# Optimization experiments

Measured on AMD Instinct MI355X. Metric: run time of the kernel, lower is better.

The kernel has to match this reference:

```python
import jax, jax.numpy as jnp
import numpy as np

DIM = 512
NUM_HEADS = 8
HEAD_DIM = DIM // NUM_HEADS
EPS = 1e-6


def setup_inputs() -> dict:
    key = jax.random.key(0)
    k_x, k_qkv, k_out, k_b = jax.random.split(key, 4)
    B, N = 8, 4096
    x = jax.random.normal(k_x, (B, N, DIM), dtype=jnp.float32)
    # nn.Linear weights stored as [out_features, in_features]; we keep [in, out] for x @ W
    s_qkv = 1.0 / np.sqrt(DIM)
    W_qkv = jax.random.uniform(k_qkv, (DIM, 3 * DIM), minval=-s_qkv, maxval=s_qkv, dtype=jnp.float32)
    W_out = jax.random.uniform(k_out, (DIM, DIM), minval=-s_qkv, maxval=s_qkv, dtype=jnp.float32)
    b_out = jax.random.uniform(k_b, (DIM,), minval=-s_qkv, maxval=s_qkv, dtype=jnp.float32)
    return {"x": x, "W_qkv": W_qkv, "W_out": W_out, "b_out": b_out}


def _feature_map(x):
    # elu(x) + 1
    return jax.nn.elu(x) + 1.0


def reference(x, W_qkv, W_out, b_out):
    B, N, C = x.shape
    H, D = NUM_HEADS, HEAD_DIM
    qkv = x @ W_qkv                              # [B, N, 3C]
    qkv = qkv.reshape(B, N, 3, H, D).transpose(2, 0, 3, 1, 4)  # [3, B, H, N, D]
    q, k, v = qkv[0], qkv[1], qkv[2]
    q_phi = _feature_map(q)                      # [B, H, N, D]
    k_phi = _feature_map(k)
    KV = jnp.einsum('bhnd,bhne->bhde', k_phi, v)  # [B, H, D, D]
    K_sum = k_phi.sum(axis=2)                     # [B, H, D]
    denom = jnp.einsum('bhnd,bhd->bhn', q_phi, K_sum)[..., None] + EPS  # [B, H, N, 1]
    out = jnp.einsum('bhnd,bhde->bhne', q_phi, KV) / denom              # [B, H, N, D]
    out = out.transpose(0, 2, 1, 3).reshape(B, N, C)
    return out @ W_out + b_out
```

## Files before the change

### kernel.cpp

```cpp
#include <hip/hip_runtime.h>
#include <stdint.h>

typedef float    f32x4 __attribute__((ext_vector_type(4)));
typedef short    s16x8 __attribute__((ext_vector_type(8)));
typedef short    s16x4 __attribute__((ext_vector_type(4)));
typedef unsigned short u16;
typedef uint32_t u32;

#define DEVINL __device__ __forceinline__

DEVINL float bf2f(u16 u) { union { u32 i; float f; } x; x.i = ((u32)u) << 16; return x.f; }
DEVINL u16 f2bf(float f) {
  union { float f; u32 i; } x; x.f = f;
  u32 i = x.i;
  return (u16)((i + 0x7FFFu + ((i >> 16) & 1u)) >> 16);
}

DEVINL void gload16(const void* g, void* l) {
  __builtin_amdgcn_global_load_lds((const __attribute__((address_space(1))) void*)g,
                                   (__attribute__((address_space(3))) void*)l,
                                   16, 0, 0);
}

__global__ __launch_bounds__(256) void k_conv_bf16(const float* __restrict__ x,
                                                   u16* __restrict__ xb, int n8) {
  int stride = gridDim.x * blockDim.x;
  for (int i = blockIdx.x * blockDim.x + threadIdx.x; i < n8; i += stride) {
    const f32x4* p = (const f32x4*)(x + (size_t)i * 8);
    f32x4 a = p[0], b = p[1];
    s16x8 o;
    o[0] = (short)f2bf(a[0]); o[1] = (short)f2bf(a[1]);
    o[2] = (short)f2bf(a[2]); o[3] = (short)f2bf(a[3]);
    o[4] = (short)f2bf(b[0]); o[5] = (short)f2bf(b[1]);
    o[6] = (short)f2bf(b[2]); o[7] = (short)f2bf(b[3]);
    *(s16x8*)(xb + (size_t)i * 8) = o;
  }
}

__global__ __launch_bounds__(256) void k_transpose_bf16(const float* __restrict__ W,
                                                        u16* __restrict__ Wt, int K, int N) {
  __shared__ __align__(16) float t[64][65];
  int nb = N >> 6;
  int tn = blockIdx.x % nb, tk = blockIdx.x / nb;
  int n0 = tn << 6, k0 = tk << 6;
  int tid = threadIdx.x;
  int cr = tid >> 4, cc = (tid & 15) << 2;
#pragma unroll
  for (int i = 0; i < 4; i++) {
    int r = cr + (i << 4);
    f32x4 v = *(const f32x4*)(W + (size_t)(k0 + r) * N + n0 + cc);
    t[r][cc] = v[0]; t[r][cc + 1] = v[1]; t[r][cc + 2] = v[2]; t[r][cc + 3] = v[3];
  }
  __syncthreads();
#pragma unroll
  for (int i = 0; i < 4; i++) {
    int nn = cr + (i << 4);
    s16x4 o;
    o[0] = (short)f2bf(t[cc    ][nn]);
    o[1] = (short)f2bf(t[cc + 1][nn]);
    o[2] = (short)f2bf(t[cc + 2][nn]);
    o[3] = (short)f2bf(t[cc + 3][nn]);
    *(s16x4*)(Wt + (size_t)(n0 + nn) * K + k0 + cc) = o;
  }
}

template <int EPI>
__global__ __launch_bounds__(512, 1) void k_gemm(
    const u16* __restrict__ A, const u16* __restrict__ Bt,
    int nbn,
    u16* __restrict__ qph, u16* __restrict__ kph, u16* __restrict__ vv,
    float* __restrict__ out, const float* __restrict__ bias) {
  __shared__ __align__(16) u16 lsA[3][256 * 32];
  __shared__ __align__(16) u16 lsB[3][256 * 32];

  int nwg = gridDim.x;
  int bx = blockIdx.x;
  int o = (bx & 7) * (nwg >> 3) + (bx >> 3);
  int bm = o / nbn, bn = o % nbn;
  int m0 = bm << 8, n0 = bn << 8;
  int tid = threadIdx.x;
  int w = tid >> 6, lane = tid & 63;
  int lnlo = lane & 15, lnhi = lane >> 4;
  int wr = w >> 2, wc = w & 3;

  const u16* gAp[2]; const u16* gBp[2]; int ldst[2];
#pragma unroll
  for (int i = 0; i < 2; i++) {
    int c = tid + i * 512;
    int row = c >> 2, ch = c & 3;
    int gch = ch ^ ((row >> 1) & 3);
    gAp[i] = A + (size_t)(m0 + row) * 512 + gch * 8;
    gBp[i] = Bt + (size_t)(n0 + row) * 512 + gch * 8;
    ldst[i] = c * 8;
  }

  int offA[8], offB[4];
#pragma unroll
  for (int f = 0; f < 8; f++) {
    int r = wr * 128 + f * 16 + lnlo;
    offA[f] = r * 32 + (lnhi ^ ((r >> 1) & 3)) * 8;
  }
#pragma unroll
  for (int f = 0; f < 4; f++) {
    int r = wc * 64 + f * 16 + lnlo;
    offB[f] = r * 32 + (lnhi ^ ((r >> 1) & 3)) * 8;
  }

  f32x4 acc[8][4] = {};

#pragma unroll
  for (int i = 0; i < 2; i++) gload16(gAp[i], &lsA[0][ldst[i]]);
#pragma unroll
  for (int i = 0; i < 2; i++) gload16(gBp[i], &lsB[0][ldst[i]]);
#pragma unroll
  for (int i = 0; i < 2; i++) gload16(gAp[i] + 32, &lsA[1][ldst[i]]);
#pragma unroll
  for (int i = 0; i < 2; i++) gload16(gBp[i] + 32, &lsB[1][ldst[i]]);
  asm volatile("s_waitcnt vmcnt(4)" ::: "memory");
  __builtin_amdgcn_s_barrier();

#pragma unroll
  for (int t = 0; t < 16; t++) {
    int buf = t % 3;
    const u16* La = &lsA[buf][0];
    const u16* Lb = &lsB[buf][0];
    int k2 = (t + 2) * 32;
    int b2 = (t + 2) % 3;

    s16x8 bf[4], af[4];
#pragma unroll
    for (int f = 0; f < 4; f++) bf[f] = *(const s16x8*)(Lb + offB[f]);
#pragma unroll
    for (int f = 0; f < 4; f++) af[f] = *(const s16x8*)(La + offA[f]);
    if (t < 14) {
#pragma unroll
      for (int i = 0; i < 2; i++) gload16(gAp[i] + k2, &lsA[b2][ldst[i]]);
    }
    __builtin_amdgcn_s_barrier();
    __builtin_amdgcn_s_setprio(1);
#pragma unroll
    for (int mf = 0; mf < 4; mf++)
#pragma unroll
      for (int nf = 0; nf < 4; nf++)
        acc[mf][nf] = __builtin_amdgcn_mfma_f32_16x16x32_bf16(af[mf], bf[nf], acc[mf][nf], 0, 0, 0);
    __builtin_amdgcn_s_setprio(0);
    __builtin_amdgcn_s_barrier();

    s16x8 af2[4];
#pragma unroll
    for (int f = 0; f < 4; f++) af2[f] = *(const s16x8*)(La + offA[4 + f]);
    if (t < 14) {
#pragma unroll
      for (int i = 0; i < 2; i++) gload16(gBp[i] + k2, &lsB[b2][ldst[i]]);
    }
    __builtin_amdgcn_s_barrier();
    __builtin_amdgcn_s_setprio(1);
#pragma unroll
    for (int mf = 0; mf < 4; mf++)
#pragma unroll
      for (int nf = 0; nf < 4; nf++)
        acc[4 + mf][nf] = __builtin_amdgcn_mfma_f32_16x16x32_bf16(af2[mf], bf[nf], acc[4 + mf][nf], 0, 0, 0);
    __builtin_amdgcn_s_setprio(0);
    if (t <= 13)      asm volatile("s_waitcnt vmcnt(4)" ::: "memory");
    else if (t == 14) asm volatile("s_waitcnt vmcnt(0)" ::: "memory");
    if (t < 15) __builtin_amdgcn_s_barrier();
  }

  int gmB = m0 + wr * 128;
  int gnB = n0 + wc * 64;
  if (EPI == 0) {
#pragma unroll
    for (int mf = 0; mf < 8; mf++) {
#pragma unroll
      for (int nf = 0; nf < 4; nf++) {
        int col = gnB + nf * 16 + lnlo;
        int sec = col >> 9;
        int hh = (col >> 6) & 7;
        int dd = col & 63;
        u16* dst = (sec == 0) ? qph : ((sec == 1) ? kph : vv);
#pragma unroll
        for (int r = 0; r < 4; r++) {
          int rowm = gmB + mf * 16 + lnhi * 4 + r;
          float val = acc[mf][nf][r];
          if (sec < 2) val = (val > 0.f) ? (val + 1.f) : __expf(val);
          int bidx = rowm >> 12, tok = rowm & 4095;
          dst[(((size_t)(bidx * 8 + hh) * 4096 + tok) << 6) + dd] = f2bf(val);
        }
      }
    }
  } else {
#pragma unroll
    for (int mf = 0; mf < 8; mf++) {
#pragma unroll
      for (int nf = 0; nf < 4; nf++) {
        int col = gnB + nf * 16 + lnlo;
        float bv = bias[col];
#pragma unroll
        for (int r = 0; r < 4; r++) {
          int rowm = gmB + mf * 16 + lnhi * 4 + r;
          out[(size_t)rowm * 512 + col] = acc[mf][nf][r] + bv;
        }
      }
    }
  }
}

__global__ __launch_bounds__(256) void k_kv(const u16* __restrict__ kphi,
                                            const u16* __restrict__ vbuf,
                                            float* __restrict__ kvpart,
                                            float* __restrict__ kspart) {
  __shared__ __align__(16) float kf[16][64];
  __shared__ __align__(16) float vf[16][64];
  int bx = blockIdx.x;
  int bh = bx >> 4, ck = bx & 15;
  int tid = threadIdx.x;
  size_t base = ((size_t)bh * 4096 + ck * 256) * 64;
  float acc[4][4] = {};
  float ks[4] = {0.f, 0.f, 0.f, 0.f};
  int dq = tid >> 4, eq = tid & 15;
  int d0 = dq * 4, e0 = eq * 4;
  int half = tid >> 7;
  int t2 = tid & 127;
  int srow = t2 >> 3, sch = t2 & 7;

  for (int step = 0; step < 16; step++) {
    {
      const u16* src = (half ? vbuf : kphi) + base + (size_t)(step * 16 + srow) * 64 + sch * 8;
      s16x8 v8 = *(const s16x8*)src;
      float* dst = (half ? &vf[0][0] : &kf[0][0]) + srow * 64 + sch * 8;
      f32x4 lo = {bf2f((u16)v8[0]), bf2f((u16)v8[1]), bf2f((u16)v8[2]), bf2f((u16)v8[3])};
      f32x4 hi = {bf2f((u16)v8[4]), bf2f((u16)v8[5]), bf2f((u16)v8[6]), bf2f((u16)v8[7])};
      *(f32x4*)dst = lo;
      *(f32x4*)(dst + 4) = hi;
    }
    __syncthreads();
#pragma unroll
    for (int tk = 0; tk < 16; tk++) {
      f32x4 kq = *(const f32x4*)&kf[tk][d0];
      f32x4 vq = *(const f32x4*)&vf[tk][e0];
#pragma unroll
      for (int i = 0; i < 4; i++)
#pragma unroll
        for (int j = 0; j < 4; j++) acc[i][j] += kq[i] * vq[j];
      if (eq == 0) {
#pragma unroll
        for (int i = 0; i < 4; i++) ks[i] += kq[i];
      }
    }
    __syncthreads();
  }
  size_t pb = (size_t)(bh * 16 + ck) * 4096;
#pragma unroll
  for (int i = 0; i < 4; i++) {
    f32x4 o = {acc[i][0], acc[i][1], acc[i][2], acc[i][3]};
    *(f32x4*)(kvpart + pb + (size_t)(d0 + i) * 64 + e0) = o;
  }
  if (eq == 0) {
    f32x4 o = {ks[0], ks[1], ks[2], ks[3]};
    *(f32x4*)(kspart + (size_t)(bh * 16 + ck) * 64 + d0) = o;
  }
}

__global__ __launch_bounds__(256) void k_kvred(const float* __restrict__ kvpart,
                                               const float* __restrict__ kspart,
                                               u16* __restrict__ kvt_sw,
                                               float* __restrict__ ksum) {
  int bh = blockIdx.x;
  int tid = threadIdx.x;
  int e = tid >> 2, d0 = (tid & 3) * 16;
  size_t pb = (size_t)bh * 16 * 4096;
#pragma unroll
  for (int dd = 0; dd < 16; dd++) {
    int d = d0 + dd;
    float s = 0.f;
#pragma unroll
    for (int c = 0; c < 16; c++) s += kvpart[pb + (size_t)c * 4096 + d * 64 + e];
    int chs = (d >> 3) ^ (e & 7);
    kvt_sw[((size_t)bh * 64 + e) * 64 + chs * 8 + (d & 7)] = f2bf(s);
  }
  if (tid < 64) {
    float s = 0.f;
#pragma unroll
    for (int c = 0; c < 16; c++) s += kspart[(size_t)bh * 1024 + c * 64 + tid];
    ksum[bh * 64 + tid] = s;
  }
}

__global__ __launch_bounds__(256, 2) void k_attnout(const u16* __restrict__ qphi,
                                                    const u16* __restrict__ kvt_sw,
                                                    const float* __restrict__ ksum,
                                                    u16* __restrict__ y) {
  __shared__ __align__(16) u16 qa[256 * 64];
  __shared__ __align__(16) u16 bb[64 * 64];
  __shared__ float ksl[64];
  __shared__ float rdnl[256];
  int bx = blockIdx.x;
  int bh = bx >> 4, tch = bx & 15;
  int b = bh >> 3, hh = bh & 7;
  int tid = threadIdx.x, w = tid >> 6, lane = tid & 63;
  int lnlo = lane & 15, lnhi = lane >> 4;
  size_t qbase = ((size_t)bh * 4096 + tch * 256) * 64;

#pragma unroll
  for (int i = 0; i < 8; i++) {
    int c = i * 256 + tid;
    int row = c >> 3, ch = c & 7;
    int gcol = (ch ^ (row & 7)) << 3;
    gload16(qphi + qbase + (size_t)row * 64 + gcol, &qa[c * 8]);
  }
#pragma unroll
  for (int i = 0; i < 2; i++) {
    int c = i * 256 + tid;
    gload16(kvt_sw + (size_t)bh * 4096 + c * 8, &bb[c * 8]);
  }
  if (tid < 64) ksl[tid] = ksum[bh * 64 + tid];
  __syncthreads();

  {
    float den = 0.f;
#pragma unroll
    for (int ch = 0; ch < 8; ch++) {
      s16x8 v8 = *(const s16x8*)&qa[tid * 64 + ((ch ^ (tid & 7)) << 3)];
#pragma unroll
      for (int j = 0; j < 8; j++) den += bf2f((u16)v8[j]) * ksl[ch * 8 + j];
    }
    rdnl[tid] = 1.f / (den + 1e-6f);
  }
  __syncthreads();

  f32x4 acc[4][4] = {};
#pragma unroll
  for (int kk = 0; kk < 2; kk++) {
    s16x8 af[4], bfr[4];
#pragma unroll
    for (int f = 0; f < 4; f++) {
      int ra = w * 64 + f * 16 + lnlo;
      int ca = (kk * 4 + lnhi) ^ (ra & 7);
      af[f] = *(const s16x8*)&qa[ra * 64 + ca * 8];
      int rb = f * 16 + lnlo;
      int cb = (kk * 4 + lnhi) ^ (rb & 7);
      bfr[f] = *(const s16x8*)&bb[rb * 64 + cb * 8];
    }
#pragma unroll
    for (int mf = 0; mf < 4; mf++)
#pragma unroll
      for (int nf = 0; nf < 4; nf++)
        acc[mf][nf] = __builtin_amdgcn_mfma_f32_16x16x32_bf16(af[mf], bfr[nf], acc[mf][nf], 0, 0, 0);
  }

  size_t yrow0 = (size_t)b * 4096 + tch * 256;
#pragma unroll
  for (int mf = 0; mf < 4; mf++) {
#pragma unroll
    for (int nf = 0; nf < 4; nf++) {
      int e = nf * 16 + lnlo;
#pragma unroll
      for (int r = 0; r < 4; r++) {
        int tl = w * 64 + mf * 16 + lnhi * 4 + r;
        float val = acc[mf][nf][r] * rdnl[tl];
        y[(yrow0 + tl) * 512 + hh * 64 + e] = f2bf(val);
      }
    }
  }
}

#define OFF_XB     ((size_t)0)
#define OFF_WQKVT  ((size_t)33554432)
#define OFF_WOUTT  ((size_t)35127296)
#define OFF_QPHI   ((size_t)35651584)
#define OFF_KPHI   ((size_t)69206016)
#define OFF_VBUF   ((size_t)102760448)
#define OFF_KVPART ((size_t)136314880)
#define OFF_KSPART ((size_t)153092096)
#define OFF_KVT    ((size_t)153354240)
#define OFF_KSUM   ((size_t)153878528)

extern "C" void kernel_launch(void* const* d_in, const int* in_sizes, int n_in,
                              void* d_out, int out_size, void* d_ws, size_t ws_size,
                              hipStream_t stream) {
  const float* x    = (const float*)d_in[0];
  const float* Wqkv = (const float*)d_in[1];
  const float* Wout = (const float*)d_in[2];
  const float* bout = (const float*)d_in[3];
  float* out = (float*)d_out;
  char* ws = (char*)d_ws;

  u16* xb     = (u16*)(ws + OFF_XB);
  u16* y      = (u16*)(ws + OFF_XB);
  u16* wqkvt  = (u16*)(ws + OFF_WQKVT);
  u16* woutt  = (u16*)(ws + OFF_WOUTT);
  u16* qphi   = (u16*)(ws + OFF_QPHI);
  u16* kphi   = (u16*)(ws + OFF_KPHI);
  u16* vbuf   = (u16*)(ws + OFF_VBUF);
  float* kvpart = (float*)(ws + OFF_KVPART);
  float* kspart = (float*)(ws + OFF_KSPART);
  u16* kvt_sw = (u16*)(ws + OFF_KVT);
  float* ksum = (float*)(ws + OFF_KSUM);

  k_conv_bf16<<<2048, 256, 0, stream>>>(x, xb, 16777216 / 8);
  k_transpose_bf16<<<(1536 / 64) * (512 / 64), 256, 0, stream>>>(Wqkv, wqkvt, 512, 1536);
  k_transpose_bf16<<<(512 / 64) * (512 / 64), 256, 0, stream>>>(Wout, woutt, 512, 512);

  k_gemm<0><<<768, 512, 0, stream>>>(xb, wqkvt, 6, qphi, kphi, vbuf, nullptr, nullptr);
  k_kv<<<64 * 16, 256, 0, stream>>>(kphi, vbuf, kvpart, kspart);
  k_kvred<<<64, 256, 0, stream>>>(kvpart, kspart, kvt_sw, ksum);
  k_attnout<<<64 * 16, 256, 0, stream>>>(qphi, kvt_sw, ksum, y);
  k_gemm<1><<<256, 512, 0, stream>>>(y, woutt, 2, nullptr, nullptr, nullptr, out, bout);
}
```

Before: 178.5 us.

## Fuse fp32-to-bf16 conversion of x into QKV GEMM loads

Removes the separate x conversion kernel and adds a dedicated QKV GEMM that loads fp32 x through registers, converts to bf16, and stores into double-buffered LDS, replacing the direct global-to-LDS triple-buffered pipeline. This avoids writing and re-reading a bf16 copy of x, but the GEMM now reads fp32 A, which is twice the bytes, and A is re-read by each of the 6 column tiles. It also uses a simpler register-staged pipeline that may overlap less well. Separately, the k_kv inner loop is restructured to batch LDS loads four rows at a time.

```diff
diff --git a/kernel.cpp b/kernel.cpp
--- a/kernel.cpp
+++ b/kernel.cpp
@@ -8,6 +8,7 @@
 typedef uint32_t u32;
 
 #define DEVINL __device__ __forceinline__
+#define CFENCE asm volatile("" ::: "memory")
 
 DEVINL float bf2f(u16 u) { union { u32 i; float f; } x; x.i = ((u32)u) << 16; return x.f; }
 DEVINL u16 f2bf(float f) {
@@ -20,21 +21,6 @@
   __builtin_amdgcn_global_load_lds((const __attribute__((address_space(1))) void*)g,
                                    (__attribute__((address_space(3))) void*)l,
                                    16, 0, 0);
-}
-
-__global__ __launch_bounds__(256) void k_conv_bf16(const float* __restrict__ x,
-                                                   u16* __restrict__ xb, int n8) {
-  int stride = gridDim.x * blockDim.x;
-  for (int i = blockIdx.x * blockDim.x + threadIdx.x; i < n8; i += stride) {
-    const f32x4* p = (const f32x4*)(x + (size_t)i * 8);
-    f32x4 a = p[0], b = p[1];
-    s16x8 o;
-    o[0] = (short)f2bf(a[0]); o[1] = (short)f2bf(a[1]);
-    o[2] = (short)f2bf(a[2]); o[3] = (short)f2bf(a[3]);
-    o[4] = (short)f2bf(b[0]); o[5] = (short)f2bf(b[1]);
-    o[6] = (short)f2bf(b[2]); o[7] = (short)f2bf(b[3]);
-    *(s16x8*)(xb + (size_t)i * 8) = o;
-  }
 }
 
 __global__ __launch_bounds__(256) void k_transpose_bf16(const float* __restrict__ W,
@@ -61,6 +47,120 @@
     o[2] = (short)f2bf(t[cc + 2][nn]);
     o[3] = (short)f2bf(t[cc + 3][nn]);
     *(s16x4*)(Wt + (size_t)(n0 + nn) * K + k0 + cc) = o;
+  }
+}
+
+__global__ __launch_bounds__(512, 1) void k_gemm1(
+    const float* __restrict__ A, const u16* __restrict__ Bt, int nbn,
+    u16* __restrict__ qph, u16* __restrict__ kph, u16* __restrict__ vv) {
+  __shared__ __align__(16) u16 lsA[2][256 * 32];
+  __shared__ __align__(16) u16 lsB[2][256 * 32];
+
+  int nwg = gridDim.x, bx = blockIdx.x;
+  int o = (bx & 7) * (nwg >> 3) + (bx >> 3);
+  int bm = o / nbn, bn = o % nbn;
+  int m0 = bm << 8, n0 = bn << 8;
+  int tid = threadIdx.x, w = tid >> 6, lane = tid & 63;
+  int lnlo = lane & 15, lnhi = lane >> 4;
+  int wr = w >> 2, wc = w & 3;
+
+  const float* gAf[2]; const u16* gBp[2]; int ldst[2];
+#pragma unroll
+  for (int i = 0; i < 2; i++) {
+    int c = tid + i * 512, row = c >> 2, ch = c & 3;
+    int gch = ch ^ ((row >> 1) & 3);
+    gAf[i] = A + (size_t)(m0 + row) * 512 + gch * 8;
+    gBp[i] = Bt + (size_t)(n0 + row) * 512 + gch * 8;
+    ldst[i] = c * 8;
+  }
+  int offA[8], offB[4];
+#pragma unroll
+  for (int f = 0; f < 8; f++) { int r = wr * 128 + f * 16 + lnlo; offA[f] = r * 32 + (lnhi ^ ((r >> 1) & 3)) * 8; }
+#pragma unroll
+  for (int f = 0; f < 4; f++) { int r = wc * 64 + f * 16 + lnlo; offB[f] = r * 32 + (lnhi ^ ((r >> 1) & 3)) * 8; }
+
+  f32x4 rA[2][2]; s16x8 rB[2];
+  f32x4 acc[8][4] = {};
+
+#pragma unroll
+  for (int i = 0; i < 2; i++) {
+    const float* s = gAf[i];
+    rA[i][0] = *(const f32x4*)s; rA[i][1] = *(const f32x4*)(s + 4);
+    rB[i] = *(const s16x8*)gBp[i];
+  }
+#pragma unroll
+  for (int i = 0; i < 2; i++) {
+    s16x8 oo;
+#pragma unroll
+    for (int j = 0; j < 4; j++) { oo[j] = (short)f2bf(rA[i][0][j]); oo[4 + j] = (short)f2bf(rA[i][1][j]); }
+    *(s16x8*)&lsA[0][ldst[i]] = oo;
+    *(s16x8*)&lsB[0][ldst[i]] = rB[i];
+  }
+  asm volatile("s_waitcnt lgkmcnt(0)" ::: "memory");
+  __builtin_amdgcn_s_barrier();
+  CFENCE;
+
+#pragma unroll
+  for (int t = 0; t < 16; t++) {
+    const int par = t & 1;
+    if (t < 15) {
+      int k1 = (t + 1) * 32;
+#pragma unroll
+      for (int i = 0; i < 2; i++) {
+        const float* s = gAf[i] + k1;
+        rA[i][0] = *(const f32x4*)s; rA[i][1] = *(const f32x4*)(s + 4);
+        rB[i] = *(const s16x8*)(gBp[i] + k1);
+      }
+    }
+    CFENCE;
+    s16x8 af[8], bf[4];
+#pragma unroll
+    for (int f = 0; f < 4; f++) bf[f] = *(const s16x8*)&lsB[par][offB[f]];
+#pragma unroll
+    for (int f = 0; f < 8; f++) af[f] = *(const s16x8*)&lsA[par][offA[f]];
+    __builtin_amdgcn_s_setprio(1);
+#pragma unroll
+    for (int mf = 0; mf < 8; mf++)
+#pragma unroll
+      for (int nf = 0; nf < 4; nf++)
+        acc[mf][nf] = __builtin_amdgcn_mfma_f32_16x16x32_bf16(af[mf], bf[nf], acc[mf][nf], 0, 0, 0);
+    __builtin_amdgcn_s_setprio(0);
+    if (t < 15) {
+#pragma unroll
+      for (int i = 0; i < 2; i++) {
+        s16x8 oo;
+#pragma unroll
+        for (int j = 0; j < 4; j++) { oo[j] = (short)f2bf(rA[i][0][j]); oo[4 + j] = (short)f2bf(rA[i][1][j]); }
+        *(s16x8*)&lsA[par ^ 1][ldst[i]] = oo;
+        *(s16x8*)&lsB[par ^ 1][ldst[i]] = rB[i];
+      }
+      asm volatile("s_waitcnt lgkmcnt(0)" ::: "memory");
+      CFENCE;
+      __builtin_amdgcn_s_barrier();
+      CFENCE;
+    }
+  }
+
+  int gmB = m0 + wr * 128;
+  int gnB = n0 + wc * 64;
+#pragma unroll
+  for (int mf = 0; mf < 8; mf++) {
+#pragma unroll
+    for (int nf = 0; nf < 4; nf++) {
+      int col = gnB + nf * 16 + lnlo;
+      int sec = col >> 9;
+      int hh = (col >> 6) & 7;
+      int dd = col & 63;
+      u16* dst = (sec == 0) ? qph : ((sec == 1) ? kph : vv);
+#pragma unroll
+      for (int r = 0; r < 4; r++) {
+        int rowm = gmB + mf * 16 + lnhi * 4 + r;
+        float val = acc[mf][nf][r];
+        if (sec < 2) val = (val > 0.f) ? (val + 1.f) : __expf(val);
+        int bidx = rowm >> 12, tok = rowm & 4095;
+        dst[(((size_t)(bidx * 8 + hh) * 4096 + tok) << 6) + dd] = f2bf(val);
+      }
+    }
   }
 }
 
@@ -168,38 +268,16 @@
 
   int gmB = m0 + wr * 128;
   int gnB = n0 + wc * 64;
-  if (EPI == 0) {
-#pragma unroll
-    for (int mf = 0; mf < 8; mf++) {
-#pragma unroll
-      for (int nf = 0; nf < 4; nf++) {
-        int col = gnB + nf * 16 + lnlo;
-        int sec = col >> 9;
-        int hh = (col >> 6) & 7;
-        int dd = col & 63;
-        u16* dst = (sec == 0) ? qph : ((sec == 1) ? kph : vv);
-#pragma unroll
-        for (int r = 0; r < 4; r++) {
-          int rowm = gmB + mf * 16 + lnhi * 4 + r;
-          float val = acc[mf][nf][r];
-          if (sec < 2) val = (val > 0.f) ? (val + 1.f) : __expf(val);
-          int bidx = rowm >> 12, tok = rowm & 4095;
-          dst[(((size_t)(bidx * 8 + hh) * 4096 + tok) << 6) + dd] = f2bf(val);
-        }
-      }
-    }
-  } else {
-#pragma unroll
-    for (int mf = 0; mf < 8; mf++) {
-#pragma unroll
-      for (int nf = 0; nf < 4; nf++) {
-        int col = gnB + nf * 16 + lnlo;
-        float bv = bias[col];
-#pragma unroll
-        for (int r = 0; r < 4; r++) {
-          int rowm = gmB + mf * 16 + lnhi * 4 + r;
-          out[(size_t)rowm * 512 + col] = acc[mf][nf][r] + bv;
-        }
+#pragma unroll
+  for (int mf = 0; mf < 8; mf++) {
+#pragma unroll
+    for (int nf = 0; nf < 4; nf++) {
+      int col = gnB + nf * 16 + lnlo;
+      float bv = bias[col];
+#pragma unroll
+      for (int r = 0; r < 4; r++) {
+        int rowm = gmB + mf * 16 + lnhi * 4 + r;
+        out[(size_t)rowm * 512 + col] = acc[mf][nf][r] + bv;
       }
     }
   }
@@ -235,16 +313,23 @@
     }
     __syncthreads();
 #pragma unroll
-    for (int tk = 0; tk < 16; tk++) {
-      f32x4 kq = *(const f32x4*)&kf[tk][d0];
-      f32x4 vq = *(const f32x4*)&vf[tk][e0];
-#pragma unroll
-      for (int i = 0; i < 4; i++)
-#pragma unroll
-        for (int j = 0; j < 4; j++) acc[i][j] += kq[i] * vq[j];
-      if (eq == 0) {
-#pragma unroll
-        for (int i = 0; i < 4; i++) ks[i] += kq[i];
+    for (int tkb = 0; tkb < 4; tkb++) {
+      f32x4 kq[4], vq[4];
+#pragma unroll
+      for (int j = 0; j < 4; j++) {
+        kq[j] = *(const f32x4*)&kf[tkb * 4 + j][d0];
+        vq[j] = *(const f32x4*)&vf[tkb * 4 + j][e0];
+      }
+#pragma unroll
+      for (int j = 0; j < 4; j++) {
+#pragma unroll
+        for (int i = 0; i < 4; i++)
+#pragma unroll
+          for (int l = 0; l < 4; l++) acc[i][l] += kq[j][i] * vq[j][l];
+        if (eq == 0) {
+#pragma unroll
+          for (int i = 0; i < 4; i++) ks[i] += kq[j][i];
+        }
       }
     }
     __syncthreads();
@@ -364,7 +449,7 @@
   }
 }
 
-#define OFF_XB     ((size_t)0)
+#define OFF_Y      ((size_t)0)
 #define OFF_WQKVT  ((size_t)33554432)
 #define OFF_WOUTT  ((size_t)35127296)
 #define OFF_QPHI   ((size_t)35651584)
@@ -385,8 +470,7 @@
   float* out = (float*)d_out;
   char* ws = (char*)d_ws;
 
-  u16* xb     = (u16*)(ws + OFF_XB);
-  u16* y      = (u16*)(ws + OFF_XB);
+  u16* y      = (u16*)(ws + OFF_Y);
   u16* wqkvt  = (u16*)(ws + OFF_WQKVT);
   u16* woutt  = (u16*)(ws + OFF_WOUTT);
   u16* qphi   = (u16*)(ws + OFF_QPHI);
@@ -397,11 +481,10 @@
   u16* kvt_sw = (u16*)(ws + OFF_KVT);
   float* ksum = (float*)(ws + OFF_KSUM);
 
-  k_conv_bf16<<<2048, 256, 0, stream>>>(x, xb, 16777216 / 8);
   k_transpose_bf16<<<(1536 / 64) * (512 / 64), 256, 0, stream>>>(Wqkv, wqkvt, 512, 1536);
   k_transpose_bf16<<<(512 / 64) * (512 / 64), 256, 0, stream>>>(Wout, woutt, 512, 512);
 
-  k_gemm<0><<<768, 512, 0, stream>>>(xb, wqkvt, 6, qphi, kphi, vbuf, nullptr, nullptr);
+  k_gemm1<<<768, 512, 0, stream>>>(x, wqkvt, 6, qphi, kphi, vbuf);
   k_kv<<<64 * 16, 256, 0, stream>>>(kphi, vbuf, kvpart, kspart);
   k_kvred<<<64, 256, 0, stream>>>(kvpart, kspart, kvt_sw, ksum);
   k_attnout<<<64 * 16, 256, 0, stream>>>(qphi, kvt_sw, ksum, y);
```

Result: slower. 197.3 us (+10.5%).

## Stage GEMM and attention epilogues through LDS for vectorized 16-byte stores

Applied to the files above, without the earlier changes.

The QKV GEMM epilogue and the attention output epilogue now write bf16 results into shared memory first. They then read them back as contiguous 8-element vectors, so each thread issues wide coalesced global stores instead of scattered 2-byte stores. The KV accumulation loop is also restructured to batch four k/v loads before the FMAs, improving instruction-level parallelism. The cost is extra LDS traffic, more barriers per row fragment, and a reliance on the per-wave ebuf region not being read by other waves. The attention epilogue synchronises only with lgkmcnt waits and no barrier, which is valid only if each wave uses just its own slice.

```diff
diff --git a/kernel.cpp b/kernel.cpp
--- a/kernel.cpp
+++ b/kernel.cpp
@@ -8,6 +8,7 @@
 typedef uint32_t u32;
 
 #define DEVINL __device__ __forceinline__
+#define CFENCE asm volatile("" ::: "memory")
 
 DEVINL float bf2f(u16 u) { union { u32 i; float f; } x; x.i = ((u32)u) << 16; return x.f; }
 DEVINL u16 f2bf(float f) {
@@ -166,29 +167,43 @@
     if (t < 15) __builtin_amdgcn_s_barrier();
   }
 
-  int gmB = m0 + wr * 128;
-  int gnB = n0 + wc * 64;
   if (EPI == 0) {
+    __syncthreads();
+    u16* ebuf = &lsA[0][0];
+    const int EROW = 272;
+    int sec = n0 >> 9;
+    u16* dstE = (sec == 0) ? qph : ((sec == 1) ? kph : vv);
+    bool isphi = (sec < 2);
+    int erow = tid >> 4;
+    int ecol = (tid & 15) << 4;
+    int rowm = m0 + ((erow >> 4) << 7) + (erow & 15);
+    int col = n0 + ecol;
+    int hh = (col >> 6) & 7, dd = col & 63;
 #pragma unroll
     for (int mf = 0; mf < 8; mf++) {
 #pragma unroll
-      for (int nf = 0; nf < 4; nf++) {
-        int col = gnB + nf * 16 + lnlo;
-        int sec = col >> 9;
-        int hh = (col >> 6) & 7;
-        int dd = col & 63;
-        u16* dst = (sec == 0) ? qph : ((sec == 1) ? kph : vv);
+      for (int nf = 0; nf < 4; nf++)
 #pragma unroll
         for (int r = 0; r < 4; r++) {
-          int rowm = gmB + mf * 16 + lnhi * 4 + r;
           float val = acc[mf][nf][r];
-          if (sec < 2) val = (val > 0.f) ? (val + 1.f) : __expf(val);
-          int bidx = rowm >> 12, tok = rowm & 4095;
-          dst[(((size_t)(bidx * 8 + hh) * 4096 + tok) << 6) + dd] = f2bf(val);
+          if (isphi) val = (val > 0.f) ? (val + 1.f) : __expf(val);
+          ebuf[(wr * 16 + lnhi * 4 + r) * EROW + wc * 64 + nf * 16 + lnlo] = f2bf(val);
         }
+      __syncthreads();
+      {
+        int rm = rowm + mf * 16;
+        int bidx = rm >> 12, tok = rm & 4095;
+        size_t base = (((size_t)(bidx * 8 + hh) * 4096 + tok) << 6) + dd;
+        s16x8 v0 = *(const s16x8*)&ebuf[erow * EROW + ecol];
+        s16x8 v1 = *(const s16x8*)&ebuf[erow * EROW + ecol + 8];
+        *(s16x8*)&dstE[base] = v0;
+        *(s16x8*)&dstE[base + 8] = v1;
       }
+      __syncthreads();
     }
   } else {
+    int gmB = m0 + wr * 128;
+    int gnB = n0 + wc * 64;
 #pragma unroll
     for (int mf = 0; mf < 8; mf++) {
 #pragma unroll
@@ -235,29 +250,36 @@
     }
     __syncthreads();
 #pragma unroll
-    for (int tk = 0; tk < 16; tk++) {
-      f32x4 kq = *(const f32x4*)&kf[tk][d0];
-      f32x4 vq = *(const f32x4*)&vf[tk][e0];
-#pragma unroll
-      for (int i = 0; i < 4; i++)
-#pragma unroll
-        for (int j = 0; j < 4; j++) acc[i][j] += kq[i] * vq[j];
-      if (eq == 0) {
-#pragma unroll
-        for (int i = 0; i < 4; i++) ks[i] += kq[i];
+    for (int tkb = 0; tkb < 4; tkb++) {
+      f32x4 kq[4], vq[4];
+#pragma unroll
+      for (int j = 0; j < 4; j++) {
+        kq[j] = *(const f32x4*)&kf[tkb * 4 + j][d0];
+        vq[j] = *(const f32x4*)&vf[tkb * 4 + j][e0];
       }
+#pragma unroll
+      for (int j = 0; j < 4; j++) {
+#pragma unroll
+        for (int i = 0; i < 4; i++)
+#pragma unroll
+          for (int l = 0; l < 4; l++) acc[i][l] += kq[j][i] * vq[j][l];
+        if (eq == 0) {
+#pragma unroll
+          for (int i = 0; i < 4; i++) ks[i] += kq[j][i];
+        }
+      }
     }
     __syncthreads();
   }
   size_t pb = (size_t)(bh * 16 + ck) * 4096;
 #pragma unroll
   for (int i = 0; i < 4; i++) {
-    f32x4 o = {acc[i][0], acc[i][1], acc[i][2], acc[i][3]};
-    *(f32x4*)(kvpart + pb + (size_t)(d0 + i) * 64 + e0) = o;
+    f32x4 oo = {acc[i][0], acc[i][1], acc[i][2], acc[i][3]};
+    *(f32x4*)(kvpart + pb + (size_t)(d0 + i) * 64 + e0) = oo;
   }
   if (eq == 0) {
-    f32x4 o = {ks[0], ks[1], ks[2], ks[3]};
-    *(f32x4*)(kspart + (size_t)(bh * 16 + ck) * 64 + d0) = o;
+    f32x4 oo = {ks[0], ks[1], ks[2], ks[3]};
+    *(f32x4*)(kspart + (size_t)(bh * 16 + ck) * 64 + d0) = oo;
   }
 }
 
@@ -348,19 +370,30 @@
         acc[mf][nf] = __builtin_amdgcn_mfma_f32_16x16x32_bf16(af[mf], bfr[nf], acc[mf][nf], 0, 0, 0);
   }
 
+  u16* ebuf = &qa[w * 4096];
+  const int AROW = 72;
+  int erow = lane >> 2, echunk = (lane & 3) << 4;
   size_t yrow0 = (size_t)b * 4096 + tch * 256;
 #pragma unroll
   for (int mf = 0; mf < 4; mf++) {
 #pragma unroll
-    for (int nf = 0; nf < 4; nf++) {
-      int e = nf * 16 + lnlo;
+    for (int nf = 0; nf < 4; nf++)
 #pragma unroll
       for (int r = 0; r < 4; r++) {
         int tl = w * 64 + mf * 16 + lnhi * 4 + r;
         float val = acc[mf][nf][r] * rdnl[tl];
-        y[(yrow0 + tl) * 512 + hh * 64 + e] = f2bf(val);
+        ebuf[(lnhi * 4 + r) * AROW + nf * 16 + lnlo] = f2bf(val);
       }
-    }
+    asm volatile("s_waitcnt lgkmcnt(0)" ::: "memory");
+    {
+      int tok = w * 64 + mf * 16 + erow;
+      size_t dst = (yrow0 + tok) * 512 + hh * 64 + echunk;
+      s16x8 v0 = *(const s16x8*)&ebuf[erow * AROW + echunk];
+      s16x8 v1 = *(const s16x8*)&ebuf[erow * AROW + echunk + 8];
+      *(s16x8*)&y[dst] = v0;
+      *(s16x8*)&y[dst + 8] = v1;
+    }
+    asm volatile("s_waitcnt lgkmcnt(0)" ::: "memory");
   }
 }
 
```

New measurement: 184.9 us. 1.04x slower.

## Store K/V transposed and compute KV partials with MFMA; merge prep kernels

Applied to the files above, without the earlier changes.

The QKV GEMM epilogue now writes phi(K) and V in a transposed [bh, d, token] layout using 8-byte vector stores. This lets the KV-accumulation kernel stage whole 64x256 tiles into swizzled LDS with direct global-to-LDS loads and compute K^T V with bf16 MFMA instead of scalar FP32 FMAs. The three prep kernels (x conversion and two weight transposes) are merged into one launch. The transposed stores are strided across tokens, which may cost some write efficiency in the GEMM epilogue.

```diff
diff --git a/kernel.cpp b/kernel.cpp
--- a/kernel.cpp
+++ b/kernel.cpp
@@ -22,28 +22,36 @@
                                    16, 0, 0);
 }
 
-__global__ __launch_bounds__(256) void k_conv_bf16(const float* __restrict__ x,
-                                                   u16* __restrict__ xb, int n8) {
-  int stride = gridDim.x * blockDim.x;
-  for (int i = blockIdx.x * blockDim.x + threadIdx.x; i < n8; i += stride) {
-    const f32x4* p = (const f32x4*)(x + (size_t)i * 8);
-    f32x4 a = p[0], b = p[1];
-    s16x8 o;
-    o[0] = (short)f2bf(a[0]); o[1] = (short)f2bf(a[1]);
-    o[2] = (short)f2bf(a[2]); o[3] = (short)f2bf(a[3]);
-    o[4] = (short)f2bf(b[0]); o[5] = (short)f2bf(b[1]);
-    o[6] = (short)f2bf(b[2]); o[7] = (short)f2bf(b[3]);
-    *(s16x8*)(xb + (size_t)i * 8) = o;
-  }
-}
-
-__global__ __launch_bounds__(256) void k_transpose_bf16(const float* __restrict__ W,
-                                                        u16* __restrict__ Wt, int K, int N) {
+__global__ __launch_bounds__(256) void k_prep(const float* __restrict__ x,
+                                              u16* __restrict__ xb,
+                                              const float* __restrict__ Wqkv,
+                                              u16* __restrict__ wqkvt,
+                                              const float* __restrict__ Wout,
+                                              u16* __restrict__ woutt) {
   __shared__ __align__(16) float t[64][65];
+  int b = blockIdx.x;
+  int tid = threadIdx.x;
+  if (b < 2048) {
+    const int n8 = 2097152;
+    int stride = 2048 * 256;
+    for (int i = b * 256 + tid; i < n8; i += stride) {
+      const f32x4* p = (const f32x4*)(x + (size_t)i * 8);
+      f32x4 a = p[0], c = p[1];
+      s16x8 o;
+      o[0] = (short)f2bf(a[0]); o[1] = (short)f2bf(a[1]);
+      o[2] = (short)f2bf(a[2]); o[3] = (short)f2bf(a[3]);
+      o[4] = (short)f2bf(c[0]); o[5] = (short)f2bf(c[1]);
+      o[6] = (short)f2bf(c[2]); o[7] = (short)f2bf(c[3]);
+      *(s16x8*)(xb + (size_t)i * 8) = o;
+    }
+    return;
+  }
+  const float* W; u16* Wt; int K, N, tb;
+  if (b < 2048 + 192) { W = Wqkv; Wt = wqkvt; K = 512; N = 1536; tb = b - 2048; }
+  else               { W = Wout; Wt = woutt; K = 512; N = 512;  tb = b - 2240; }
   int nb = N >> 6;
-  int tn = blockIdx.x % nb, tk = blockIdx.x / nb;
+  int tn = tb % nb, tk = tb / nb;
   int n0 = tn << 6, k0 = tk << 6;
-  int tid = threadIdx.x;
   int cr = tid >> 4, cc = (tid & 15) << 2;
 #pragma unroll
   for (int i = 0; i < 4; i++) {
@@ -68,7 +76,7 @@
 __global__ __launch_bounds__(512, 1) void k_gemm(
     const u16* __restrict__ A, const u16* __restrict__ Bt,
     int nbn,
-    u16* __restrict__ qph, u16* __restrict__ kph, u16* __restrict__ vv,
+    u16* __restrict__ qph, u16* __restrict__ kphT, u16* __restrict__ vT,
     float* __restrict__ out, const float* __restrict__ bias) {
   __shared__ __align__(16) u16 lsA[3][256 * 32];
   __shared__ __align__(16) u16 lsB[3][256 * 32];
@@ -169,22 +177,45 @@
   int gmB = m0 + wr * 128;
   int gnB = n0 + wc * 64;
   if (EPI == 0) {
-#pragma unroll
-    for (int mf = 0; mf < 8; mf++) {
-#pragma unroll
-      for (int nf = 0; nf < 4; nf++) {
-        int col = gnB + nf * 16 + lnlo;
-        int sec = col >> 9;
-        int hh = (col >> 6) & 7;
-        int dd = col & 63;
-        u16* dst = (sec == 0) ? qph : ((sec == 1) ? kph : vv);
-#pragma unroll
-        for (int r = 0; r < 4; r++) {
-          int rowm = gmB + mf * 16 + lnhi * 4 + r;
-          float val = acc[mf][nf][r];
-          if (sec < 2) val = (val > 0.f) ? (val + 1.f) : __expf(val);
-          int bidx = rowm >> 12, tok = rowm & 4095;
-          dst[(((size_t)(bidx * 8 + hh) * 4096 + tok) << 6) + dd] = f2bf(val);
+    int sec = n0 >> 9;
+    if (sec == 0) {
+#pragma unroll
+      for (int mf = 0; mf < 8; mf++) {
+#pragma unroll
+        for (int nf = 0; nf < 4; nf++) {
+          int col = gnB + nf * 16 + lnlo;
+          int hh = (col >> 6) & 7;
+          int dd = col & 63;
+#pragma unroll
+          for (int r = 0; r < 4; r++) {
+            int rowm = gmB + mf * 16 + lnhi * 4 + r;
+            float val = acc[mf][nf][r];
+            val = (val > 0.f) ? (val + 1.f) : __expf(val);
+            int bidx = rowm >> 12, tok = rowm & 4095;
+            qph[(((size_t)(bidx * 8 + hh) * 4096 + tok) << 6) + dd] = f2bf(val);
+          }
+        }
+      }
+    } else {
+      u16* dstT = (sec == 1) ? kphT : vT;
+      bool isphi = (sec == 1);
+#pragma unroll
+      for (int mf = 0; mf < 8; mf++) {
+        int rowm = gmB + mf * 16 + lnhi * 4;
+        int bidx = rowm >> 12, tok = rowm & 4095;
+#pragma unroll
+        for (int nf = 0; nf < 4; nf++) {
+          int col = gnB + nf * 16 + lnlo;
+          int hh = (col >> 6) & 7;
+          int dd = col & 63;
+          s16x4 o4;
+#pragma unroll
+          for (int r = 0; r < 4; r++) {
+            float val = acc[mf][nf][r];
+            if (isphi) val = (val > 0.f) ? (val + 1.f) : __expf(val);
+            o4[r] = (short)f2bf(val);
+          }
+          *(s16x4*)&dstT[((size_t)(bidx * 8 + hh) * 64 + dd) * 4096 + tok] = o4;
         }
       }
     }
@@ -205,60 +236,72 @@
   }
 }
 
-__global__ __launch_bounds__(256) void k_kv(const u16* __restrict__ kphi,
-                                            const u16* __restrict__ vbuf,
-                                            float* __restrict__ kvpart,
-                                            float* __restrict__ kspart) {
-  __shared__ __align__(16) float kf[16][64];
-  __shared__ __align__(16) float vf[16][64];
+__global__ __launch_bounds__(256, 2) void k_kv(const u16* __restrict__ kphT,
+                                               const u16* __restrict__ vT,
+                                               float* __restrict__ kvpart,
+                                               float* __restrict__ kspart) {
+  __shared__ __align__(16) u16 lsK[64 * 256];
+  __shared__ __align__(16) u16 lsV[64 * 256];
+  __shared__ float red[4][64];
   int bx = blockIdx.x;
   int bh = bx >> 4, ck = bx & 15;
-  int tid = threadIdx.x;
-  size_t base = ((size_t)bh * 4096 + ck * 256) * 64;
-  float acc[4][4] = {};
-  float ks[4] = {0.f, 0.f, 0.f, 0.f};
-  int dq = tid >> 4, eq = tid & 15;
-  int d0 = dq * 4, e0 = eq * 4;
-  int half = tid >> 7;
-  int t2 = tid & 127;
-  int srow = t2 >> 3, sch = t2 & 7;
-
-  for (int step = 0; step < 16; step++) {
-    {
-      const u16* src = (half ? vbuf : kphi) + base + (size_t)(step * 16 + srow) * 64 + sch * 8;
-      s16x8 v8 = *(const s16x8*)src;
-      float* dst = (half ? &vf[0][0] : &kf[0][0]) + srow * 64 + sch * 8;
-      f32x4 lo = {bf2f((u16)v8[0]), bf2f((u16)v8[1]), bf2f((u16)v8[2]), bf2f((u16)v8[3])};
-      f32x4 hi = {bf2f((u16)v8[4]), bf2f((u16)v8[5]), bf2f((u16)v8[6]), bf2f((u16)v8[7])};
-      *(f32x4*)dst = lo;
-      *(f32x4*)(dst + 4) = hi;
-    }
-    __syncthreads();
-#pragma unroll
-    for (int tk = 0; tk < 16; tk++) {
-      f32x4 kq = *(const f32x4*)&kf[tk][d0];
-      f32x4 vq = *(const f32x4*)&vf[tk][e0];
-#pragma unroll
-      for (int i = 0; i < 4; i++)
-#pragma unroll
-        for (int j = 0; j < 4; j++) acc[i][j] += kq[i] * vq[j];
-      if (eq == 0) {
-#pragma unroll
-        for (int i = 0; i < 4; i++) ks[i] += kq[i];
-      }
-    }
-    __syncthreads();
-  }
+  int tid = threadIdx.x, w = tid >> 6, lane = tid & 63;
+  int lnlo = lane & 15, lnhi = lane >> 4;
+  size_t gbase = (size_t)bh * 64 * 4096 + ck * 256;
+
+#pragma unroll
+  for (int i = 0; i < 8; i++) {
+    int c = tid + i * 256;
+    int row = c >> 5, ch = c & 31;
+    int gch = ch ^ (row & 31);
+    gload16(kphT + gbase + (size_t)row * 4096 + gch * 8, &lsK[c * 8]);
+  }
+#pragma unroll
+  for (int i = 0; i < 8; i++) {
+    int c = tid + i * 256;
+    int row = c >> 5, ch = c & 31;
+    int gch = ch ^ (row & 31);
+    gload16(vT + gbase + (size_t)row * 4096 + gch * 8, &lsV[c * 8]);
+  }
+  asm volatile("s_waitcnt vmcnt(0)" ::: "memory");
+  __builtin_amdgcn_s_barrier();
+
+  f32x4 acc[4] = {{0.f, 0.f, 0.f, 0.f}, {0.f, 0.f, 0.f, 0.f},
+                  {0.f, 0.f, 0.f, 0.f}, {0.f, 0.f, 0.f, 0.f}};
+  int rb = w * 16 + lnlo;
+#pragma unroll
+  for (int kk = 0; kk < 8; kk++) {
+    s16x8 bfr = *(const s16x8*)&lsV[rb * 256 + ((kk * 4 + lnhi) ^ (rb & 31)) * 8];
+#pragma unroll
+    for (int mf = 0; mf < 4; mf++) {
+      int ra = mf * 16 + lnlo;
+      s16x8 af = *(const s16x8*)&lsK[ra * 256 + ((kk * 4 + lnhi) ^ (ra & 31)) * 8];
+      acc[mf] = __builtin_amdgcn_mfma_f32_16x16x32_bf16(af, bfr, acc[mf], 0, 0, 0);
+    }
+  }
+
+  {
+    int d = tid & 63, q = tid >> 6;
+    float s = 0.f;
+#pragma unroll
+    for (int j = 0; j < 8; j++) {
+      s16x8 v8 = *(const s16x8*)&lsK[d * 256 + (q * 8 + j) * 8];
+#pragma unroll
+      for (int e = 0; e < 8; e++) s += bf2f((u16)v8[e]);
+    }
+    red[q][d] = s;
+  }
+  __syncthreads();
+
   size_t pb = (size_t)(bh * 16 + ck) * 4096;
 #pragma unroll
-  for (int i = 0; i < 4; i++) {
-    f32x4 o = {acc[i][0], acc[i][1], acc[i][2], acc[i][3]};
-    *(f32x4*)(kvpart + pb + (size_t)(d0 + i) * 64 + e0) = o;
-  }
-  if (eq == 0) {
-    f32x4 o = {ks[0], ks[1], ks[2], ks[3]};
-    *(f32x4*)(kspart + (size_t)(bh * 16 + ck) * 64 + d0) = o;
-  }
+  for (int mf = 0; mf < 4; mf++)
+#pragma unroll
+    for (int r = 0; r < 4; r++)
+      kvpart[pb + (size_t)(mf * 16 + lnhi * 4 + r) * 64 + (w * 16 + lnlo)] = acc[mf][r];
+  if (tid < 64)
+    kspart[(size_t)(bh * 16 + ck) * 64 + tid] =
+        red[0][tid] + red[1][tid] + red[2][tid] + red[3][tid];
 }
 
 __global__ __launch_bounds__(256) void k_kvred(const float* __restrict__ kvpart,
@@ -390,19 +433,17 @@
   u16* wqkvt  = (u16*)(ws + OFF_WQKVT);
   u16* woutt  = (u16*)(ws + OFF_WOUTT);
   u16* qphi   = (u16*)(ws + OFF_QPHI);
-  u16* kphi   = (u16*)(ws + OFF_KPHI);
-  u16* vbuf   = (u16*)(ws + OFF_VBUF);
+  u16* kphT   = (u16*)(ws + OFF_KPHI);
+  u16* vT     = (u16*)(ws + OFF_VBUF);
   float* kvpart = (float*)(ws + OFF_KVPART);
   float* kspart = (float*)(ws + OFF_KSPART);
   u16* kvt_sw = (u16*)(ws + OFF_KVT);
   float* ksum = (float*)(ws + OFF_KSUM);
 
-  k_conv_bf16<<<2048, 256, 0, stream>>>(x, xb, 16777216 / 8);
-  k_transpose_bf16<<<(1536 / 64) * (512 / 64), 256, 0, stream>>>(Wqkv, wqkvt, 512, 1536);
-  k_transpose_bf16<<<(512 / 64) * (512 / 64), 256, 0, stream>>>(Wout, woutt, 512, 512);
-
-  k_gemm<0><<<768, 512, 0, stream>>>(xb, wqkvt, 6, qphi, kphi, vbuf, nullptr, nullptr);
-  k_kv<<<64 * 16, 256, 0, stream>>>(kphi, vbuf, kvpart, kspart);
+  k_prep<<<2304, 256, 0, stream>>>(x, xb, Wqkv, wqkvt, Wout, woutt);
+
+  k_gemm<0><<<768, 512, 0, stream>>>(xb, wqkvt, 6, qphi, kphT, vT, nullptr, nullptr);
+  k_kv<<<64 * 16, 256, 0, stream>>>(kphT, vT, kvpart, kspart);
   k_kvred<<<64, 256, 0, stream>>>(kvpart, kspart, kvt_sw, ksum);
   k_attnout<<<64 * 16, 256, 0, stream>>>(qphi, kvt_sw, ksum, y);
   k_gemm<1><<<256, 512, 0, stream>>>(y, woutt, 2, nullptr, nullptr, nullptr, out, bout);
```

After: 159.3 us. 10.7% less time.
